# Optimization experiments

Measured on AMD Instinct MI355X. Metric: run time of the kernel, lower is better.

The kernel has to match this reference:

```python
import jax, jax.numpy as jnp
import numpy as np

EPS_FEAT = 1.0 + 1e-4   # feature_map offset: elu(x) + 1.0 + 0.0001
EPS_DEN = 1e-6


def setup_inputs() -> dict:
    key = jax.random.key(0)
    k1, k2, k3 = jax.random.split(key, 3)
    B, L, D = 4, 4096, 1024
    x = jax.random.normal(k1, (B, L, D), dtype=jnp.float32)
    # torch Linear-style init scale ~ 1/sqrt(fan_in)
    W_qkv = jax.random.normal(k2, (D, 3 * D), dtype=jnp.float32) / np.sqrt(D)
    b_qkv = jnp.zeros((3 * D,), dtype=jnp.float32)
    W_out = jax.random.normal(k3, (D, D), dtype=jnp.float32) / np.sqrt(D)
    b_out = jnp.zeros((D,), dtype=jnp.float32)
    return {"x": x, "W_qkv": W_qkv, "b_qkv": b_qkv, "W_out": W_out, "b_out": b_out}


def _linear_attention(x, W_qkv, b_qkv, W_out, b_out, num_heads=16):
    B, L, D = x.shape
    H = num_heads
    E = D // H

    qkv = x @ W_qkv + b_qkv                       # (B, L, 3D)
    q, k, v = jnp.split(qkv, 3, axis=-1)
    q = q.reshape(B, L, H, E)
    k = k.reshape(B, L, H, E)
    v = v.reshape(B, L, H, E)

    q = jax.nn.elu(q * (E ** -0.5)) + EPS_FEAT    # scale BEFORE feature map (as in source)
    k = jax.nn.elu(k) + EPS_FEAT

    # Causal linear attention via recurrence over L; math identical to
    # cumsum of k \otimes v outer products, but never materializes (B,L,H,E,E).
    qL = jnp.moveaxis(q, 1, 0)                    # (L, B, H, E)
    kL = jnp.moveaxis(k, 1, 0)
    vL = jnp.moveaxis(v, 1, 0)

    kv0 = jnp.zeros((B, H, E, E), dtype=x.dtype)
    ks0 = jnp.zeros((B, H, E), dtype=x.dtype)

    def step(carry, qkv_t):
        kv_s, k_s = carry
        q_t, k_t, v_t = qkv_t                     # each (B, H, E)
        kv_s = kv_s + jnp.einsum('bhe,bhf->bhef', k_t, v_t)
        k_s = k_s + k_t
        num = jnp.einsum('bhe,bhef->bhf', q_t, kv_s)           # (B, H, E)
        den = jnp.einsum('bhe,bhe->bh', q_t, k_s)[..., None] + EPS_DEN
        return (kv_s, k_s), num / den

    _, out = jax.lax.scan(step, (kv0, ks0), (qL, kL, vL))       # out: (L, B, H, E)
    out = jnp.moveaxis(out, 0, 1).reshape(B, L, D)
    # dropout is identity in eval mode
    return out @ W_out + b_out


def reference(x, W_qkv, b_qkv, W_out, b_out):
    return _linear_attention(x, W_qkv, b_qkv, W_out, b_out)
```

## Files before the change

### kernel.cpp

```cpp
#include <hip/hip_runtime.h>
#include <hip/hip_bf16.h>
#include <stdint.h>

#define B_ 4
#define L_ 4096
#define D_ 1024
#define H_ 16
#define E_ 64
#define M_ (B_*L_)
#define N1_ (3*D_)
#define CHK 128
#define NC (L_/CHK)
#define BH (B_*H_)

#define EPS_FEAT 1.0001f
#define EPS_DEN 1e-6f

typedef __attribute__((ext_vector_type(4))) float f32x4;
typedef __attribute__((ext_vector_type(8))) short bf16x8;

__device__ __forceinline__ unsigned short f2bf(float x) {
    union { float f; unsigned int u; } v; v.f = x;
    unsigned int r = v.u + 0x7FFFu + ((v.u >> 16) & 1u);
    return (unsigned short)(r >> 16);
}

__device__ __forceinline__ void gload_lds16(const unsigned short* g, unsigned short* l) {
    __builtin_amdgcn_global_load_lds(
        (const __attribute__((address_space(1))) unsigned int*)(const void*)g,
        (__attribute__((address_space(3))) unsigned int*)(void*)l,
        16, 0, 0);
}


__global__ __launch_bounds__(256) void prep(const float* __restrict__ x,
                                            const float* __restrict__ W0,
                                            const float* __restrict__ W1,
                                            unsigned short* __restrict__ xb,
                                            unsigned short* __restrict__ T0,
                                            unsigned short* __restrict__ T1) {
    __shared__ float tile[32][33];
    int bid = blockIdx.x, t = threadIdx.x;
    if (bid < 16384) {
        int i4 = bid * 256 + t;
        float4 v = ((const float4*)x)[i4];
        unsigned int lo = (unsigned int)f2bf(v.x) | ((unsigned int)f2bf(v.y) << 16);
        unsigned int hi = (unsigned int)f2bf(v.z) | ((unsigned int)f2bf(v.w) << 16);
        ((uint2*)xb)[i4] = make_uint2(lo, hi);
        return;
    }
    const float* W; unsigned short* WT; int N, nb, kb;
    if (bid < 16384 + 3072) {
        int idx = bid - 16384;
        W = W0; WT = T0; N = N1_;
        nb = (idx % 96) * 32; kb = (idx / 96) * 32;
    } else {
        int idx = bid - 16384 - 3072;
        W = W1; WT = T1; N = D_;
        nb = (idx % 32) * 32; kb = (idx / 32) * 32;
    }
    int tx = t & 31, ty = t >> 5;
#pragma unroll
    for (int j = 0; j < 4; ++j)
        tile[ty + 8*j][tx] = W[(size_t)(kb + ty + 8*j) * N + nb + tx];
    __syncthreads();
#pragma unroll
    for (int j = 0; j < 4; ++j) {
        int nl = ty + 8*j;
        WT[(size_t)(nb + nl) * D_ + kb + tx] = f2bf(tile[tx][nl]);
    }
}


template<int MODE, int KDIM, int NDIM>
__global__ __launch_bounds__(512, 2) void gemm256(
    const unsigned short* __restrict__ A,
    const unsigned short* __restrict__ BT,
    const float* __restrict__ bias,
    float* __restrict__ outF,
    unsigned short* __restrict__ qf,
    unsigned short* __restrict__ kf,
    unsigned short* __restrict__ vf)
{
    __shared__ __align__(16) unsigned short smem[65536];

    const int t = threadIdx.x, lane = t & 63, w = t >> 6;
    const int wr = w >> 2, wc = w & 3;

    const int nwgx = NDIM / 256;
    const int nwg = nwgx * (M_ / 256);
    const int bid0 = blockIdx.y * nwgx + blockIdx.x;
    const int swz = (bid0 & 7) * (nwg >> 3) + (bid0 >> 3);
    const int m0 = (swz / nwgx) * 256, n0 = (swz % nwgx) * 256;
    const int lr = lane & 15, lg = lane >> 4;

    auto stage = [&](int T, int ab, int h) {
        unsigned short* base = smem + (T & 1) * 32768 + ab * 16384 + h * 8192;
        const unsigned short* src = ab ? BT : A;
        const int boff = (ab ? n0 : m0) + h * 128;
        const int kt = T * 64;
#pragma unroll
        for (int i = 0; i < 2; ++i) {
            int c = i * 512 + t;
            int rowl = c >> 3, s = c & 7;
            int col = ((s ^ (rowl & 7)) << 3);
            gload_lds16(src + (size_t)(boff + rowl) * KDIM + kt + col, &base[c * 8]);
        }
    };

    f32x4 acc[8][4] = {};

    auto rdA = [&](const unsigned short* Ab, int m, int ks) {
        int row = wr * 128 + m * 16 + lr;
        int slot = (ks * 4 + lg) ^ (row & 7);
        return *(const bf16x8*)&Ab[row * 64 + slot * 8];
    };
    auto rdB = [&](const unsigned short* Bb, int n, int ks) {
        int row = wc * 64 + n * 16 + lr;
        int slot = (ks * 4 + lg) ^ (row & 7);
        return *(const bf16x8*)&Bb[row * 64 + slot * 8];
    };

#define PHASE_PRE() \
    __builtin_amdgcn_s_barrier(); \
    asm volatile("s_waitcnt lgkmcnt(0)" ::: "memory"); \
    __builtin_amdgcn_sched_barrier(0); \
    __builtin_amdgcn_s_setprio(1);
#define PHASE_POST() \
    __builtin_amdgcn_s_setprio(0);

    auto tile = [&](int T, bool s1, bool s2) {
        const unsigned short* Ab = smem + (T & 1) * 32768;
        const unsigned short* Bb = Ab + 16384;
        bf16x8 a0[4][2], a1[4][2], bq[4][2];
#pragma unroll
        for (int m = 0; m < 4; ++m) { a0[m][0] = rdA(Ab, m, 0); a0[m][1] = rdA(Ab, m, 1); }
#pragma unroll
        for (int n = 0; n < 4; ++n) { bq[n][0] = rdB(Bb, n, 0); bq[n][1] = rdB(Bb, n, 1); }
        if (s1) { stage(T + 1, 0, 0); stage(T + 1, 0, 1); }
        PHASE_PRE();
#pragma unroll
        for (int m = 0; m < 4; ++m)
#pragma unroll
            for (int n = 0; n < 4; ++n) {
                acc[m][n] = __builtin_amdgcn_mfma_f32_16x16x32_bf16(a0[m][0], bq[n][0], acc[m][n], 0, 0, 0);
                acc[m][n] = __builtin_amdgcn_mfma_f32_16x16x32_bf16(a0[m][1], bq[n][1], acc[m][n], 0, 0, 0);
            }
        PHASE_POST();
#pragma unroll
        for (int m = 0; m < 4; ++m) { a1[m][0] = rdA(Ab, 4+m, 0); a1[m][1] = rdA(Ab, 4+m, 1); }
        if (s2) { stage(T + 2, 1, 0); stage(T + 2, 1, 1); }
        PHASE_PRE();
#pragma unroll
        for (int m = 0; m < 4; ++m)
#pragma unroll
            for (int n = 0; n < 4; ++n) {
                acc[4+m][n] = __builtin_amdgcn_mfma_f32_16x16x32_bf16(a1[m][0], bq[n][0], acc[4+m][n], 0, 0, 0);
                acc[4+m][n] = __builtin_amdgcn_mfma_f32_16x16x32_bf16(a1[m][1], bq[n][1], acc[4+m][n], 0, 0, 0);
            }
        PHASE_POST();
    };

    constexpr int NT = KDIM / 64;
    stage(0, 0, 0); stage(0, 0, 1); stage(0, 1, 0); stage(0, 1, 1);
    stage(1, 1, 0); stage(1, 1, 1);
    asm volatile("s_waitcnt vmcnt(4)" ::: "memory");
    __builtin_amdgcn_s_barrier();
    __builtin_amdgcn_sched_barrier(0);

    for (int T = 0; T < NT - 2; ++T) {
        tile(T, true, true);
        asm volatile("s_waitcnt vmcnt(4)" ::: "memory");
        __builtin_amdgcn_s_barrier();
        __builtin_amdgcn_sched_barrier(0);
    }
    tile(NT - 2, true, false);
    asm volatile("s_waitcnt vmcnt(0)" ::: "memory");
    __builtin_amdgcn_s_barrier();
    __builtin_amdgcn_sched_barrier(0);
    tile(NT - 1, false, false);
    __syncthreads();

    if (MODE == 0) {
        unsigned short* cbf = smem;
        const bool isQ = (n0 < D_), isK = (n0 >= D_ && n0 < 2*D_);
        const float scale = isQ ? 0.125f : 1.0f;
        unsigned short* buf = isQ ? qf : (isK ? kf : vf);
        const int b = m0 >> 12, l0 = m0 & 4095;
        const int h0 = (n0 & 1023) >> 6;
#pragma unroll
        for (int p = 0; p < 2; ++p) {
            if (wr == p) {
#pragma unroll
                for (int n = 0; n < 4; ++n) {
                    int cl = wc*64 + n*16 + lr;
                    float bv = bias[n0 + cl];
#pragma unroll
                    for (int m = 0; m < 8; ++m)
#pragma unroll
                        for (int q = 0; q < 4; ++q) {
                            int rl = m*16 + lg*4 + q;
                            float val = (acc[m][n][q] + bv) * scale;
                            float fv = (isQ || isK)
                                       ? ((val > 0.f ? val : __expf(val) - 1.f) + EPS_FEAT)
                                       : val;
                            cbf[rl * 264 + cl] = f2bf(fv);
                        }
                }
            }
            __syncthreads();
#pragma unroll
            for (int hh = 0; hh < 4; ++hh) {
                unsigned short* dst = buf + (((size_t)(b * H_ + h0 + hh)) * L_ + l0 + p*128) * E_;
#pragma unroll
                for (int i = 0; i < 2; ++i) {
                    int c = i*512 + t, row = c >> 3, ch = c & 7;
                    uint4 v = *(const uint4*)&cbf[row * 264 + hh*64 + ch*8];
                    *(uint4*)&dst[row * 64 + ch*8] = v;
                }
            }
            __syncthreads();
        }
    } else {
        float* cfl = (float*)smem;
#pragma unroll
        for (int p = 0; p < 4; ++p) {
            if (wr == (p >> 1)) {
                int mbase = (p & 1) * 4;
#pragma unroll
                for (int n = 0; n < 4; ++n) {
                    int cl = wc*64 + n*16 + lr;
                    float bv = bias[n0 + cl];
#pragma unroll
                    for (int mm = 0; mm < 4; ++mm)
#pragma unroll
                        for (int q = 0; q < 4; ++q) {
                            int rl = mm*16 + lg*4 + q;
                            cfl[rl * 260 + cl] = acc[mbase + mm][n][q] + bv;
                        }
                }
            }
            __syncthreads();
#pragma unroll
            for (int i = 0; i < 8; ++i) {
                int c = i*512 + t, row = c >> 6, ch = c & 63;
                float4 v = *(const float4*)&cfl[row * 260 + ch*4];
                *(float4*)&outF[(size_t)(m0 + p*64 + row) * NDIM + n0 + ch*4] = v;
            }
            __syncthreads();
        }
    }
#undef PHASE_PRE
#undef PHASE_POST
}


__global__ __launch_bounds__(256) void chunk_kv(
    const unsigned short* __restrict__ kf, const unsigned short* __restrict__ vf,
    float* __restrict__ kvout, float* __restrict__ ksout)
{
    constexpr int LDK = 136;
    __shared__ unsigned short Kt[64 * LDK];
    __shared__ unsigned short Vt[80 * LDK];

    int t = threadIdx.x, lane = t & 63, w = t >> 6;
    int bid = blockIdx.x;
    const unsigned short* kp = kf + (size_t)bid * CHK * E_;
    const unsigned short* vp = vf + (size_t)bid * CHK * E_;

#pragma unroll
    for (int it = 0; it < 4; ++it) {
        int s = it * 256 + t;
        int rl = s >> 3, e0 = (s & 7) << 3;
        uint4 kv8 = *(const uint4*)(kp + s * 8);
        uint4 vv8 = *(const uint4*)(vp + s * 8);
        unsigned int kw[4] = {kv8.x, kv8.y, kv8.z, kv8.w};
        unsigned int vw[4] = {vv8.x, vv8.y, vv8.z, vv8.w};
#pragma unroll
        for (int jw = 0; jw < 4; ++jw) {
            Kt[(e0 + 2*jw    ) * LDK + rl] = (unsigned short)(kw[jw] & 0xFFFF);
            Kt[(e0 + 2*jw + 1) * LDK + rl] = (unsigned short)(kw[jw] >> 16);
            Vt[(e0 + 2*jw    ) * LDK + rl] = (unsigned short)(vw[jw] & 0xFFFF);
            Vt[(e0 + 2*jw + 1) * LDK + rl] = (unsigned short)(vw[jw] >> 16);
        }
    }
    if (t < 128) Vt[64 * LDK + t] = 0x3F80;
    for (int i = t; i < 15 * LDK; i += 256) Vt[65 * LDK + i] = 0;
    __syncthreads();

    int lr = lane & 15, lg = lane >> 4;
    f32x4 acc[4] = {};
    f32x4 accE[4] = {};
#pragma unroll
    for (int ks = 0; ks < 4; ++ks) {
        bf16x8 a = *(const bf16x8*)&Vt[(w*16 + lr) * LDK + ks*32 + lg*8];
#pragma unroll
        for (int n = 0; n < 4; ++n) {
            bf16x8 b = *(const bf16x8*)&Kt[(n*16 + lr) * LDK + ks*32 + lg*8];
            acc[n] = __builtin_amdgcn_mfma_f32_16x16x32_bf16(a, b, acc[n], 0, 0, 0);
        }
    }
    if (w == 0) {
#pragma unroll
        for (int ks = 0; ks < 4; ++ks) {
            bf16x8 a = *(const bf16x8*)&Vt[(64 + lr) * LDK + ks*32 + lg*8];
#pragma unroll
            for (int n = 0; n < 4; ++n) {
                bf16x8 b = *(const bf16x8*)&Kt[(n*16 + lr) * LDK + ks*32 + lg*8];
                accE[n] = __builtin_amdgcn_mfma_f32_16x16x32_bf16(a, b, accE[n], 0, 0, 0);
            }
        }
    }
    float* kvo = kvout + (size_t)bid * E_ * E_;
#pragma unroll
    for (int n = 0; n < 4; ++n)
#pragma unroll
        for (int q = 0; q < 4; ++q) {
            int f = w*16 + lg*4 + q, e = n*16 + lr;
            kvo[f * 64 + e] = acc[n][q];
        }
    if (w == 0 && lg == 0) {
#pragma unroll
        for (int n = 0; n < 4; ++n)
            ksout[(size_t)bid * 64 + n*16 + lr] = accE[n][0];
    }
}


__global__ __launch_bounds__(256) void prefix_kv(
    const float4* __restrict__ kv, const float* __restrict__ ks,
    uint2* __restrict__ kvb, unsigned short* __restrict__ ksb)
{
    int bh = blockIdx.y, part = blockIdx.x, t = threadIdx.x;
    int idx = part * 256 + t;
    float4 st = make_float4(0.f, 0.f, 0.f, 0.f);
    for (int c = 0; c < NC; ++c) {
        float4 tmp = kv[((size_t)bh * NC + c) * 1024 + idx];
        kvb[((size_t)bh * NC + c) * 1024 + idx] = make_uint2(
            (unsigned int)f2bf(st.x) | ((unsigned int)f2bf(st.y) << 16),
            (unsigned int)f2bf(st.z) | ((unsigned int)f2bf(st.w) << 16));
        st.x += tmp.x; st.y += tmp.y; st.z += tmp.z; st.w += tmp.w;
    }
    if (part == 0 && t < 64) {
        float s0 = 0.f;
        for (int c = 0; c < NC; ++c) {
            float tmp = ks[((size_t)bh * NC + c) * 64 + t];
            ksb[((size_t)bh * NC + c) * 64 + t] = f2bf(s0);
            s0 += tmp;
        }
    }
}


__global__ __launch_bounds__(256, 2) void attn_out(
    const unsigned short* __restrict__ qf, const unsigned short* __restrict__ kf,
    const unsigned short* __restrict__ vf, const unsigned short* __restrict__ kvb,
    const unsigned short* __restrict__ ksb, unsigned short* __restrict__ attn)
{
    constexpr int LK = 72;
    constexpr int LV = 136;
    __shared__ unsigned short Ks[128 * LK];
    __shared__ unsigned short Vt[64 * LV];
    __shared__ unsigned short Ss[128 * LV];

    int t = threadIdx.x, lane = t & 63, w = t >> 6;
    int bid = blockIdx.x;
    int bh = bid >> 5, c = bid & 31;
    const unsigned short* qp = qf + (size_t)bid * CHK * E_;
    const unsigned short* kp = kf + (size_t)bid * CHK * E_;
    const unsigned short* vp = vf + (size_t)bid * CHK * E_;
    const unsigned short* kvp = kvb + (size_t)bid * 4096;

    int lr = lane & 15, lg = lane >> 4;
    const int jsel[2] = {w, 7 - w};

    bf16x8 aq[2][2];
#pragma unroll
    for (int mi = 0; mi < 2; ++mi)
#pragma unroll
        for (int ks = 0; ks < 2; ++ks)
            aq[mi][ks] = *(const bf16x8*)(qp + (jsel[mi]*16 + lr) * 64 + ks*32 + lg*8);

#pragma unroll
    for (int it = 0; it < 4; ++it) {
        int s = it * 256 + t;
        int r = s >> 3, e0 = (s & 7) << 3;
        uint4 kv = *(const uint4*)(kp + s * 8);
        uint4 vv = *(const uint4*)(vp + s * 8);
        *(uint4*)&Ks[r * LK + e0] = kv;
        unsigned int vw[4] = {vv.x, vv.y, vv.z, vv.w};
#pragma unroll
        for (int jw = 0; jw < 4; ++jw) {
            Vt[(e0 + 2*jw    ) * LV + r] = (unsigned short)(vw[jw] & 0xFFFF);
            Vt[(e0 + 2*jw + 1) * LV + r] = (unsigned short)(vw[jw] >> 16);
        }
    }
    bf16x8 zfrag = {0,0,0,0,0,0,0,0};
    bf16x8 bone = zfrag, bks[2] = {zfrag, zfrag};
    if (lr == 0) {
#pragma unroll
        for (int j = 0; j < 8; ++j) bone[j] = (short)0x3F80;
        bks[0] = *(const bf16x8*)&ksb[(size_t)bid * 64 + lg*8];
        bks[1] = *(const bf16x8*)&ksb[(size_t)bid * 64 + 32 + lg*8];
    }
    __syncthreads();

#pragma unroll
    for (int mi = 0; mi < 2; ++mi) {
        int j = jsel[mi];
        int rbase = j * 16;
        int jbmax = j | 1;
        for (int jb = 0; jb <= jbmax; ++jb) {
            if (jb <= j) {
                f32x4 sacc = {};
                bf16x8 b0 = *(const bf16x8*)&Ks[(jb*16 + lr) * LK + lg*8];
                bf16x8 b1 = *(const bf16x8*)&Ks[(jb*16 + lr) * LK + 32 + lg*8];
                sacc = __builtin_amdgcn_mfma_f32_16x16x32_bf16(aq[mi][0], b0, sacc, 0, 0, 0);
                sacc = __builtin_amdgcn_mfma_f32_16x16x32_bf16(aq[mi][1], b1, sacc, 0, 0, 0);
#pragma unroll
                for (int q = 0; q < 4; ++q) {
                    int r = rbase + lg*4 + q;
                    int jj = jb*16 + lr;
                    Ss[r * LV + jj] = (jj <= r) ? f2bf(sacc[q]) : (unsigned short)0;
                }
            } else {
#pragma unroll
                for (int q = 0; q < 4; ++q) {
                    int r = rbase + lg*4 + q;
                    Ss[r * LV + jb*16 + lr] = 0;
                }
            }
        }
    }

    f32x4 oacc[2][5] = {};
#pragma unroll
    for (int mi = 0; mi < 2; ++mi) {
        int j = jsel[mi];
        int rbase = j * 16;
#pragma unroll
        for (int ks = 0; ks < 2; ++ks) {
            bf16x8 a = aq[mi][ks];
#pragma unroll
            for (int n = 0; n < 4; ++n) {
                bf16x8 b = *(const bf16x8*)&kvp[(n*16 + lr) * 64 + ks*32 + lg*8];
                oacc[mi][n] = __builtin_amdgcn_mfma_f32_16x16x32_bf16(a, b, oacc[mi][n], 0, 0, 0);
            }
            oacc[mi][4] = __builtin_amdgcn_mfma_f32_16x16x32_bf16(a, bks[ks], oacc[mi][4], 0, 0, 0);
        }
        for (int ks = 0; ks <= (j >> 1); ++ks) {
            bf16x8 a = *(const bf16x8*)&Ss[(rbase + lr) * LV + ks*32 + lg*8];
#pragma unroll
            for (int n = 0; n < 4; ++n) {
                bf16x8 b = *(const bf16x8*)&Vt[(n*16 + lr) * LV + ks*32 + lg*8];
                oacc[mi][n] = __builtin_amdgcn_mfma_f32_16x16x32_bf16(a, b, oacc[mi][n], 0, 0, 0);
            }
            oacc[mi][4] = __builtin_amdgcn_mfma_f32_16x16x32_bf16(a, bone, oacc[mi][4], 0, 0, 0);
        }
    }

    int b_idx = bh >> 4, h_idx = bh & 15;
#pragma unroll
    for (int mi = 0; mi < 2; ++mi) {
        int rbase = jsel[mi] * 16;
        float den[4];
#pragma unroll
        for (int q = 0; q < 4; ++q)
            den[q] = __shfl(oacc[mi][4][q], lane & 48, 64) + EPS_DEN;
#pragma unroll
        for (int n = 0; n < 4; ++n) {
#pragma unroll
            for (int q = 0; q < 4; ++q) {
                int r = rbase + lg*4 + q;
                int lpos = c * CHK + r;
                int col = n*16 + lr;
                size_t dst = ((size_t)b_idx * L_ + lpos) * D_ + h_idx * 64 + col;
                attn[dst] = f2bf(oacc[mi][n][q] / den[q]);
            }
        }
    }
}


extern "C" void kernel_launch(void* const* d_in, const int* in_sizes, int n_in,
                              void* d_out, int out_size, void* d_ws, size_t ws_size,
                              hipStream_t stream)
{
    const float* x    = (const float*)d_in[0];
    const float* Wqkv = (const float*)d_in[1];
    const float* bqkv = (const float*)d_in[2];
    const float* Wout = (const float*)d_in[3];
    const float* bout = (const float*)d_in[4];
    float* out = (float*)d_out;

    char* ws = (char*)d_ws;
    size_t off = 0;
    auto alloc = [&](size_t bytes) { void* p = ws + off; off += (bytes + 255) & ~(size_t)255; return p; };
    unsigned short* xb  = (unsigned short*)alloc((size_t)M_ * D_ * 2);
    unsigned short* WqT = (unsigned short*)alloc((size_t)N1_ * D_ * 2);
    unsigned short* WoT = (unsigned short*)alloc((size_t)D_ * D_ * 2);
    unsigned short* qfb = (unsigned short*)alloc((size_t)M_ * D_ * 2);
    unsigned short* kfb = (unsigned short*)alloc((size_t)M_ * D_ * 2);
    unsigned short* vfb = (unsigned short*)alloc((size_t)M_ * D_ * 2);
    float* kvw = (float*)alloc((size_t)BH * NC * E_ * E_ * 4);
    float* ksw = (float*)alloc((size_t)BH * NC * E_ * 4);
    unsigned short* kvb = (unsigned short*)alloc((size_t)BH * NC * E_ * E_ * 2);
    unsigned short* ksb = (unsigned short*)alloc((size_t)BH * NC * E_ * 2);
    unsigned short* attn = xb;

    prep<<<16384 + 3072 + 1024, 256, 0, stream>>>(x, Wqkv, Wout, xb, WqT, WoT);

    gemm256<0, D_, N1_><<<dim3(N1_ / 256, M_ / 256), 512, 0, stream>>>(
        xb, WqT, bqkv, nullptr, qfb, kfb, vfb);

    chunk_kv<<<BH * NC, 256, 0, stream>>>(kfb, vfb, kvw, ksw);
    prefix_kv<<<dim3(4, BH), 256, 0, stream>>>((const float4*)kvw, ksw, (uint2*)kvb, ksb);
    attn_out<<<BH * NC, 256, 0, stream>>>(qfb, kfb, vfb, kvb, ksb, attn);

    gemm256<1, D_, D_><<<dim3(D_ / 256, M_ / 256), 512, 0, stream>>>(
        attn, WoT, bout, out, nullptr, nullptr, nullptr);
}
```

Before: 239.9 us.

## Merge GEMM tile phases into one barrier and store chunk KV as bf16

The GEMM inner tile now uses a single barrier/waitcnt per tile instead of two. It issues both next-tile stage loads before the MFMA block and keeps high priority across the whole tile, which cuts synchronization overhead. Separately, chunk_kv writes per-chunk KV states as bf16 rather than fp32, halving that intermediate's traffic into prefix_kv. The cost is bf16 rounding of per-chunk sums before accumulation, and an LDS read of the second A half that is no longer fenced by a barrier.

```diff
diff --git a/kernel.cpp b/kernel.cpp
--- a/kernel.cpp
+++ b/kernel.cpp
@@ -121,24 +121,20 @@
         return *(const bf16x8*)&Bb[row * 64 + slot * 8];
     };
 
-#define PHASE_PRE() \
-    __builtin_amdgcn_s_barrier(); \
-    asm volatile("s_waitcnt lgkmcnt(0)" ::: "memory"); \
-    __builtin_amdgcn_sched_barrier(0); \
-    __builtin_amdgcn_s_setprio(1);
-#define PHASE_POST() \
-    __builtin_amdgcn_s_setprio(0);
-
     auto tile = [&](int T, bool s1, bool s2) {
         const unsigned short* Ab = smem + (T & 1) * 32768;
         const unsigned short* Bb = Ab + 16384;
-        bf16x8 a0[4][2], a1[4][2], bq[4][2];
+        bf16x8 a0[4][2], bq[4][2];
 #pragma unroll
         for (int m = 0; m < 4; ++m) { a0[m][0] = rdA(Ab, m, 0); a0[m][1] = rdA(Ab, m, 1); }
 #pragma unroll
         for (int n = 0; n < 4; ++n) { bq[n][0] = rdB(Bb, n, 0); bq[n][1] = rdB(Bb, n, 1); }
         if (s1) { stage(T + 1, 0, 0); stage(T + 1, 0, 1); }
-        PHASE_PRE();
+        __builtin_amdgcn_s_barrier();
+        asm volatile("s_waitcnt lgkmcnt(0)" ::: "memory");
+        __builtin_amdgcn_sched_barrier(0);
+        __builtin_amdgcn_s_setprio(1);
+        if (s2) { stage(T + 2, 1, 0); stage(T + 2, 1, 1); }
 #pragma unroll
         for (int m = 0; m < 4; ++m)
 #pragma unroll
@@ -146,11 +142,9 @@
                 acc[m][n] = __builtin_amdgcn_mfma_f32_16x16x32_bf16(a0[m][0], bq[n][0], acc[m][n], 0, 0, 0);
                 acc[m][n] = __builtin_amdgcn_mfma_f32_16x16x32_bf16(a0[m][1], bq[n][1], acc[m][n], 0, 0, 0);
             }
-        PHASE_POST();
+        bf16x8 a1[4][2];
 #pragma unroll
         for (int m = 0; m < 4; ++m) { a1[m][0] = rdA(Ab, 4+m, 0); a1[m][1] = rdA(Ab, 4+m, 1); }
-        if (s2) { stage(T + 2, 1, 0); stage(T + 2, 1, 1); }
-        PHASE_PRE();
 #pragma unroll
         for (int m = 0; m < 4; ++m)
 #pragma unroll
@@ -158,7 +152,7 @@
                 acc[4+m][n] = __builtin_amdgcn_mfma_f32_16x16x32_bf16(a1[m][0], bq[n][0], acc[4+m][n], 0, 0, 0);
                 acc[4+m][n] = __builtin_amdgcn_mfma_f32_16x16x32_bf16(a1[m][1], bq[n][1], acc[4+m][n], 0, 0, 0);
             }
-        PHASE_POST();
+        __builtin_amdgcn_s_setprio(0);
     };
 
     constexpr int NT = KDIM / 64;
@@ -250,14 +244,12 @@
             __syncthreads();
         }
     }
-#undef PHASE_PRE
-#undef PHASE_POST
 }
 
 
 __global__ __launch_bounds__(256) void chunk_kv(
     const unsigned short* __restrict__ kf, const unsigned short* __restrict__ vf,
-    float* __restrict__ kvout, float* __restrict__ ksout)
+    unsigned short* __restrict__ kvout, float* __restrict__ ksout)
 {
     constexpr int LDK = 136;
     __shared__ unsigned short Kt[64 * LDK];
@@ -311,13 +303,13 @@
             }
         }
     }
-    float* kvo = kvout + (size_t)bid * E_ * E_;
+    unsigned short* kvo = kvout + (size_t)bid * E_ * E_;
 #pragma unroll
     for (int n = 0; n < 4; ++n)
 #pragma unroll
         for (int q = 0; q < 4; ++q) {
             int f = w*16 + lg*4 + q, e = n*16 + lr;
-            kvo[f * 64 + e] = acc[n][q];
+            kvo[f * 64 + e] = f2bf(acc[n][q]);
         }
     if (w == 0 && lg == 0) {
 #pragma unroll
@@ -328,18 +320,23 @@
 
 
 __global__ __launch_bounds__(256) void prefix_kv(
-    const float4* __restrict__ kv, const float* __restrict__ ks,
+    const uint2* __restrict__ kvin, const float* __restrict__ ks,
     uint2* __restrict__ kvb, unsigned short* __restrict__ ksb)
 {
     int bh = blockIdx.y, part = blockIdx.x, t = threadIdx.x;
     int idx = part * 256 + t;
-    float4 st = make_float4(0.f, 0.f, 0.f, 0.f);
+    float st0 = 0.f, st1 = 0.f, st2 = 0.f, st3 = 0.f;
     for (int c = 0; c < NC; ++c) {
-        float4 tmp = kv[((size_t)bh * NC + c) * 1024 + idx];
-        kvb[((size_t)bh * NC + c) * 1024 + idx] = make_uint2(
-            (unsigned int)f2bf(st.x) | ((unsigned int)f2bf(st.y) << 16),
-            (unsigned int)f2bf(st.z) | ((unsigned int)f2bf(st.w) << 16));
-        st.x += tmp.x; st.y += tmp.y; st.z += tmp.z; st.w += tmp.w;
+        size_t o = ((size_t)bh * NC + c) * 1024 + idx;
+        uint2 tmp = kvin[o];
+        kvb[o] = make_uint2(
+            (unsigned int)f2bf(st0) | ((unsigned int)f2bf(st1) << 16),
+            (unsigned int)f2bf(st2) | ((unsigned int)f2bf(st3) << 16));
+        union { unsigned int u; float f; } cv;
+        cv.u = (tmp.x & 0xFFFFu) << 16; st0 += cv.f;
+        cv.u = tmp.x & 0xFFFF0000u;     st1 += cv.f;
+        cv.u = (tmp.y & 0xFFFFu) << 16; st2 += cv.f;
+        cv.u = tmp.y & 0xFFFF0000u;     st3 += cv.f;
     }
     if (part == 0 && t < 64) {
         float s0 = 0.f;
@@ -502,7 +499,7 @@
     unsigned short* qfb = (unsigned short*)alloc((size_t)M_ * D_ * 2);
     unsigned short* kfb = (unsigned short*)alloc((size_t)M_ * D_ * 2);
     unsigned short* vfb = (unsigned short*)alloc((size_t)M_ * D_ * 2);
-    float* kvw = (float*)alloc((size_t)BH * NC * E_ * E_ * 4);
+    unsigned short* kvw = (unsigned short*)alloc((size_t)BH * NC * E_ * E_ * 2);
     float* ksw = (float*)alloc((size_t)BH * NC * E_ * 4);
     unsigned short* kvb = (unsigned short*)alloc((size_t)BH * NC * E_ * E_ * 2);
     unsigned short* ksb = (unsigned short*)alloc((size_t)BH * NC * E_ * 2);
@@ -514,7 +511,7 @@
         xb, WqT, bqkv, nullptr, qfb, kfb, vfb);
 
     chunk_kv<<<BH * NC, 256, 0, stream>>>(kfb, vfb, kvw, ksw);
-    prefix_kv<<<dim3(4, BH), 256, 0, stream>>>((const float4*)kvw, ksw, (uint2*)kvb, ksb);
+    prefix_kv<<<dim3(4, BH), 256, 0, stream>>>((const uint2*)kvw, ksw, (uint2*)kvb, ksb);
     attn_out<<<BH * NC, 256, 0, stream>>>(qfb, kfb, vfb, kvb, ksb, attn);
 
     gemm256<1, D_, D_><<<dim3(D_ / 256, M_ / 256), 512, 0, stream>>>(
```

Result: no change. 240.4 us (+0.2%).
